# Performance work log

Hardware: AMD Instinct MI355X
Metric: run time of the kernel (lower is better)

The kernel has to match this reference:

```python
import jax, jax.numpy as jnp
import numpy as np

BN_EPS = 1e-5

def conv1x1(x, w, b):
    # x: [B,C,H,W], w: [O,C], b: [O]
    return jnp.einsum('bchw,oc->bohw', x, w) + b[None, :, None, None]

def bn_inf(x, gamma, beta, mean, var):
    inv = gamma / jnp.sqrt(var + BN_EPS)
    return (x - mean[None, :, None, None]) * inv[None, :, None, None] + beta[None, :, None, None]

def setup_inputs() -> dict:
    key = jax.random.key(0)
    ks = jax.random.split(key, 24)
    B, Fg, Fl, Fi = 8, 256, 256, 64
    H = W = 64
    c8 = Fi // 8
    d = {}
    d['g'] = jax.random.normal(ks[0], (B, Fg, H, W), jnp.float32)
    d['x'] = jax.random.normal(ks[1], (B, Fl, H, W), jnp.float32)
    # W_g: conv1x1 + BN
    d['Wg_w'] = jax.random.normal(ks[2], (Fi, Fg), jnp.float32) * (1.0 / np.sqrt(Fg))
    d['Wg_b'] = jax.random.normal(ks[3], (Fi,), jnp.float32) * 0.02
    d['bng_gamma'] = jax.random.uniform(ks[4], (Fi,), jnp.float32, 0.5, 1.5)
    d['bng_beta'] = jax.random.normal(ks[5], (Fi,), jnp.float32) * 0.1
    d['bng_mean'] = jax.random.normal(ks[6], (Fi,), jnp.float32) * 0.1
    d['bng_var'] = jax.random.uniform(ks[7], (Fi,), jnp.float32, 0.5, 1.5)
    # W_x: conv1x1 + BN
    d['Wx_w'] = jax.random.normal(ks[8], (Fi, Fl), jnp.float32) * (1.0 / np.sqrt(Fl))
    d['Wx_b'] = jax.random.normal(ks[9], (Fi,), jnp.float32) * 0.02
    d['bnx_gamma'] = jax.random.uniform(ks[10], (Fi,), jnp.float32, 0.5, 1.5)
    d['bnx_beta'] = jax.random.normal(ks[11], (Fi,), jnp.float32) * 0.1
    d['bnx_mean'] = jax.random.normal(ks[12], (Fi,), jnp.float32) * 0.1
    d['bnx_var'] = jax.random.uniform(ks[13], (Fi,), jnp.float32, 0.5, 1.5)
    # psi: conv1x1 (Fi->1) + BN(1) + sigmoid
    d['psi_w'] = jax.random.normal(ks[14], (1, Fi), jnp.float32) * (1.0 / np.sqrt(Fi))
    d['psi_b'] = jax.random.normal(ks[15], (1,), jnp.float32) * 0.02
    d['bnp_gamma'] = jax.random.uniform(ks[16], (1,), jnp.float32, 0.5, 1.5)
    d['bnp_beta'] = jax.random.normal(ks[17], (1,), jnp.float32) * 0.1
    d['bnp_mean'] = jax.random.normal(ks[18], (1,), jnp.float32) * 0.1
    d['bnp_var'] = jax.random.uniform(ks[19], (1,), jnp.float32, 0.5, 1.5)
    # PAM convs
    d['pb_w'] = jax.random.normal(ks[20], (c8, Fi), jnp.float32) * (1.0 / np.sqrt(Fi))
    d['pb_b'] = jnp.zeros((c8,), jnp.float32)
    d['pc_w'] = jax.random.normal(ks[21], (c8, Fi), jnp.float32) * (1.0 / np.sqrt(Fi))
    d['pc_b'] = jnp.zeros((c8,), jnp.float32)
    d['pd_w'] = jax.random.normal(ks[22], (Fi, Fi), jnp.float32) * (1.0 / np.sqrt(Fi))
    d['pd_b'] = jnp.zeros((Fi,), jnp.float32)
    # scalar gates (torch inits to 0; use small nonzero to exercise the path)
    d['alpha'] = jax.random.normal(ks[23], (1,), jnp.float32) * 0.05
    d['cam_beta'] = jax.random.normal(jax.random.fold_in(key, 99), (1,), jnp.float32) * 0.05
    return d

def _cam(psi, cam_beta):
    B, C, H, W = psi.shape
    feat = psi.reshape(B, C, H * W)                       # [B,C,HW]
    att = jnp.einsum('bcn,bdn->bcd', feat, feat)          # [B,C,C]
    att_new = jnp.max(att, axis=-1, keepdims=True) - att  # max-subtract trick
    att = jax.nn.softmax(att_new, axis=-1)
    out = jnp.einsum('bcd,bdn->bcn', att, feat).reshape(B, C, H, W)
    return cam_beta[0] * out + psi

def _pam(psi, pb_w, pb_b, pc_w, pc_b, pd_w, pd_b, alpha):
    B, C, H, W = psi.shape
    HW = H * W
    fb = conv1x1(psi, pb_w, pb_b).reshape(B, -1, HW)      # [B,C/8,HW]
    fc = conv1x1(psi, pc_w, pc_b).reshape(B, -1, HW)      # [B,C/8,HW]
    energy = jnp.einsum('bki,bkj->bij', fb, fc)           # [B,HW,HW]
    att = jax.nn.softmax(energy, axis=-1)
    fd = conv1x1(psi, pd_w, pd_b).reshape(B, C, HW)       # [B,C,HW]
    out = jnp.einsum('bcj,bij->bci', fd, att).reshape(B, C, H, W)
    return alpha[0] * out + psi

def reference(g, x, Wg_w, Wg_b, bng_gamma, bng_beta, bng_mean, bng_var,
              Wx_w, Wx_b, bnx_gamma, bnx_beta, bnx_mean, bnx_var,
              psi_w, psi_b, bnp_gamma, bnp_beta, bnp_mean, bnp_var,
              pb_w, pb_b, pc_w, pc_b, pd_w, pd_b, alpha, cam_beta):
    g1 = bn_inf(conv1x1(g, Wg_w, Wg_b), bng_gamma, bng_beta, bng_mean, bng_var)
    x1 = bn_inf(conv1x1(x, Wx_w, Wx_b), bnx_gamma, bnx_beta, bnx_mean, bnx_var)
    psi = jax.nn.relu(g1 + x1)                            # [B,F_int,H,W]
    cam = _cam(psi, cam_beta)
    pam = _pam(psi, pb_w, pb_b, pc_w, pc_b, pd_w, pd_b, alpha)
    gate = bn_inf(conv1x1(cam * pam, psi_w, psi_b), bnp_gamma, bnp_beta, bnp_mean, bnp_var)
    da = jax.nn.sigmoid(gate)                             # [B,1,H,W]
    return x * da
```

## Files before the change

### kernel.cpp

```cpp
#include <hip/hip_runtime.h>
#include <hip/hip_bf16.h>
#include <math.h>

#define BB 8
#define CIN 256
#define FI 64
#define HW 4096
#define C8 8
#define EPS 1e-5f

typedef __attribute__((ext_vector_type(8))) short bf16x8;
typedef __attribute__((ext_vector_type(4))) float f32x4;
typedef unsigned short u16;

static __device__ __forceinline__ u16 f2b(float x) {
    unsigned u = __builtin_bit_cast(unsigned, x);
    return (u16)((u + 0x8000u) >> 16);
}
static __device__ __forceinline__ unsigned pk2(float a, float b) {
    unsigned ua = __builtin_bit_cast(unsigned, a);
    unsigned ub = __builtin_bit_cast(unsigned, b);
    return ((ua + 0x8000u) >> 16) | ((ub + 0x8000u) & 0xffff0000u);
}
static __device__ __forceinline__ float b2f(u16 v) {
    return __builtin_bit_cast(float, ((unsigned)v) << 16);
}

__global__ __launch_bounds__(256) void k_prep(
    const float* __restrict__ Wg, const float* __restrict__ Wgb,
    const float* __restrict__ gg, const float* __restrict__ gbeta,
    const float* __restrict__ gm, const float* __restrict__ gv,
    const float* __restrict__ Wx, const float* __restrict__ Wxb,
    const float* __restrict__ xg, const float* __restrict__ xbeta,
    const float* __restrict__ xm, const float* __restrict__ xv,
    const float* __restrict__ pbw, const float* __restrict__ pbb,
    const float* __restrict__ pcw, const float* __restrict__ pcb,
    const float* __restrict__ pdw, const float* __restrict__ pdb,
    u16* __restrict__ Wp, float* __restrict__ Cp,
    u16* __restrict__ Wcat, float* __restrict__ bcat)
{
    const int gid = blockIdx.x * 256 + threadIdx.x;
    for (int idx = gid; idx < FI * 512; idx += 4096) {
        int o = idx >> 9, k = idx & 511;
        float s, w;
        if (k < 256) { s = gg[o] * rsqrtf(gv[o] + EPS); w = Wg[o * 256 + k]; }
        else         { s = xg[o] * rsqrtf(xv[o] + EPS); w = Wx[o * 256 + k - 256]; }
        Wp[idx] = f2b(w * s);
    }
    for (int idx = gid; idx < 80 * 64; idx += 4096) {
        int row = idx >> 6, col = idx & 63;
        float w;
        if (row < 8)       w = pbw[row * 64 + col];
        else if (row < 16) w = pcw[(row - 8) * 64 + col];
        else               w = pdw[(row - 16) * 64 + col];
        Wcat[idx] = f2b(w);
    }
    if (blockIdx.x == 0) {
        int tid = threadIdx.x;
        if (tid < FI) {
            float ig = gg[tid] * rsqrtf(gv[tid] + EPS);
            float ix = xg[tid] * rsqrtf(xv[tid] + EPS);
            Cp[tid] = (Wgb[tid] - gm[tid]) * ig + gbeta[tid]
                    + (Wxb[tid] - xm[tid]) * ix + xbeta[tid];
        }
        if (tid >= 64 && tid < 144) {
            int r = tid - 64;
            bcat[r] = (r < 8) ? pbb[r] : (r < 16 ? pcb[r - 8] : pdb[r - 16]);
        }
    }
}

__global__ __launch_bounds__(256) void k_psi(
    const float* __restrict__ g, const float* __restrict__ x,
    const u16* __restrict__ Wp, const float* __restrict__ Cp,
    const u16* __restrict__ Wcat, const float* __restrict__ bcat,
    u16* __restrict__ psiB, u16* __restrict__ psiLo,
    u16* __restrict__ fbcT, u16* __restrict__ fdB)
{
    const int tid  = threadIdx.x;
    const int lane = tid & 63;
    const int w    = tid >> 6;
    const int n    = lane & 15;
    const int quad = lane >> 4;
    const int b    = blockIdx.y;
    const int p0   = blockIdx.x * 64;

    __shared__ u16 InT[64][72];
    __shared__ u16 Tbc[64][16];

    f32x4 acc[4];
#pragma unroll
    for (int mt = 0; mt < 4; ++mt) acc[mt] = (f32x4){0.f, 0.f, 0.f, 0.f};

    for (int kc = 0; kc < 8; ++kc) {
        const float* src = (kc < 4) ? g : x;
        const int ch0 = (kc & 3) * 64;
        __syncthreads();
#pragma unroll
        for (int r = 0; r < 4; ++r) {
            int ch = (tid >> 4) + r * 16;
            int px = (tid & 15) * 4;
            float4 v = *(const float4*)&src[((size_t)b * CIN + ch0 + ch) * HW + p0 + px];
            InT[px][ch]     = f2b(v.x);
            InT[px + 1][ch] = f2b(v.y);
            InT[px + 2][ch] = f2b(v.z);
            InT[px + 3][ch] = f2b(v.w);
        }
        __syncthreads();
#pragma unroll
        for (int ks = 0; ks < 2; ++ks) {
            const int kglob = kc * 64 + ks * 32;
            bf16x8 bfrag = *(const bf16x8*)&InT[w * 16 + n][ks * 32 + quad * 8];
#pragma unroll
            for (int mt = 0; mt < 4; ++mt) {
                bf16x8 af = *(const bf16x8*)&Wp[(mt * 16 + n) * 512 + kglob + quad * 8];
                acc[mt] = __builtin_amdgcn_mfma_f32_16x16x32_bf16(
                              af, bfrag, acc[mt], 0, 0, 0);
            }
        }
    }

    float pv[4][4];
#pragma unroll
    for (int mt = 0; mt < 4; ++mt)
#pragma unroll
        for (int r = 0; r < 4; ++r) {
            int c = mt * 16 + quad * 4 + r;
            float v = acc[mt][r] + Cp[c];
            v = v > 0.f ? v : 0.f;
            pv[mt][r] = v;
            u16 hb = f2b(v);
            size_t idx = ((size_t)b * FI + c) * HW + p0 + w * 16 + n;
            psiB[idx]  = hb;
            psiLo[idx] = f2b(v - b2f(hb));
        }
    __syncthreads();
#pragma unroll
    for (int mt = 0; mt < 4; ++mt) {
        *(unsigned*)&InT[w * 16 + n][mt * 16 + quad * 4]     = pk2(pv[mt][0], pv[mt][1]);
        *(unsigned*)&InT[w * 16 + n][mt * 16 + quad * 4 + 2] = pk2(pv[mt][2], pv[mt][3]);
    }
    __syncthreads();

    f32x4 facc[5];
#pragma unroll
    for (int nt = 0; nt < 5; ++nt) facc[nt] = (f32x4){0.f, 0.f, 0.f, 0.f};
#pragma unroll
    for (int ks = 0; ks < 2; ++ks) {
        bf16x8 af = *(const bf16x8*)&InT[w * 16 + n][ks * 32 + quad * 8];
#pragma unroll
        for (int nt = 0; nt < 5; ++nt) {
            bf16x8 bf = *(const bf16x8*)&Wcat[(nt * 16 + n) * FI + ks * 32 + quad * 8];
            facc[nt] = __builtin_amdgcn_mfma_f32_16x16x32_bf16(af, bf, facc[nt], 0, 0, 0);
        }
    }
    __syncthreads();

    {
        float bias = bcat[n];
#pragma unroll
        for (int r = 0; r < 4; ++r)
            Tbc[w * 16 + quad * 4 + r][n] = f2b(facc[0][r] + bias);
    }
#pragma unroll
    for (int nt = 1; nt < 5; ++nt) {
        int ch = (nt - 1) * 16 + n;
        float bias = bcat[nt * 16 + n];
        *(unsigned*)&InT[ch][w * 16 + quad * 4]     = pk2(facc[nt][0] + bias, facc[nt][1] + bias);
        *(unsigned*)&InT[ch][w * 16 + quad * 4 + 2] = pk2(facc[nt][2] + bias, facc[nt][3] + bias);
    }
    __syncthreads();
    {
        int row = tid >> 2, part = tid & 3;
        uint2 v = *(const uint2*)&Tbc[row][part * 4];
        *(uint2*)&fbcT[((size_t)b * HW + p0 + row) * 16 + part * 4] = v;
    }
#pragma unroll
    for (int rep = 0; rep < 2; ++rep) {
        int t = rep * 256 + tid;
        int ch = t >> 3, seg = t & 7;
        bf16x8 v = *(const bf16x8*)&InT[ch][seg * 8];
        *(bf16x8*)&fdB[((size_t)b * FI + ch) * HW + p0 + seg * 8] = v;
    }
}

__global__ __launch_bounds__(256) void k_gram(
    const u16* __restrict__ psiB, const u16* __restrict__ psiLo,
    float* __restrict__ Gp)
{
    const int tid  = threadIdx.x;
    const int lane = tid & 63;
    const int w    = tid >> 6;
    const int n    = lane & 15;
    const int quad = lane >> 4;
    const int s    = blockIdx.x;
    const int b    = blockIdx.y;

    f32x4 acc[4];
#pragma unroll
    for (int nt = 0; nt < 4; ++nt) acc[nt] = (f32x4){0.f, 0.f, 0.f, 0.f};

    for (int ks = 0; ks < 4; ++ks) {
        const int k0 = s * 128 + ks * 32;
        const size_t ra = ((size_t)b * FI + w * 16 + n) * HW + k0 + quad * 8;
        bf16x8 ah = *(const bf16x8*)&psiB[ra];
        bf16x8 al = *(const bf16x8*)&psiLo[ra];
#pragma unroll
        for (int nt = 0; nt < 4; ++nt) {
            const size_t rb = ((size_t)b * FI + nt * 16 + n) * HW + k0 + quad * 8;
            bf16x8 bh = *(const bf16x8*)&psiB[rb];
            bf16x8 bl = *(const bf16x8*)&psiLo[rb];
            acc[nt] = __builtin_amdgcn_mfma_f32_16x16x32_bf16(ah, bh, acc[nt], 0, 0, 0);
            acc[nt] = __builtin_amdgcn_mfma_f32_16x16x32_bf16(ah, bl, acc[nt], 0, 0, 0);
            acc[nt] = __builtin_amdgcn_mfma_f32_16x16x32_bf16(al, bh, acc[nt], 0, 0, 0);
        }
    }
#pragma unroll
    for (int nt = 0; nt < 4; ++nt)
#pragma unroll
        for (int r = 0; r < 4; ++r) {
            int i = w * 16 + quad * 4 + r;
            Gp[(((size_t)s * 8 + b) * 64 + i) * 64 + nt * 16 + n] = acc[nt][r];
        }
}

__global__ __launch_bounds__(256) void k_camsm(
    const float* __restrict__ Gp, float* __restrict__ att)
{
    const int tid = threadIdx.x, d = tid & 63, ty = tid >> 6;
    const int b = blockIdx.x, grp = blockIdx.y;
#pragma unroll 1
    for (int rr = 0; rr < 4; ++rr) {
        int i = grp * 16 + ty * 4 + rr;
        float gsum = 0.f;
#pragma unroll 1
        for (int s = 0; s < 32; ++s) gsum += Gp[(((size_t)s * 8 + b) * 64 + i) * 64 + d];
        float M = gsum;
#pragma unroll
        for (int msk = 1; msk < 64; msk <<= 1) M = fmaxf(M, __shfl_xor(M, msk));
        float a = M - gsum;
        float m2 = a;
#pragma unroll
        for (int msk = 1; msk < 64; msk <<= 1) m2 = fmaxf(m2, __shfl_xor(m2, msk));
        float p = __expf(a - m2);
        float ssum = p;
#pragma unroll
        for (int msk = 1; msk < 64; msk <<= 1) ssum += __shfl_xor(ssum, msk);
        att[((size_t)b * 64 + i) * 64 + d] = p / ssum;
    }
}

__global__ __launch_bounds__(256) void k_pam(
    const u16* __restrict__ fbcT, const u16* __restrict__ fdB,
    u16* __restrict__ Opart, float* __restrict__ ml)
{
    const int tid  = threadIdx.x;
    const int lane = tid & 63;
    const int w    = tid >> 6;
    const int n    = lane & 15;
    const int quad = lane >> 4;
    const int b    = blockIdx.x;
    const int i0   = blockIdx.y * 64;
    const int p    = blockIdx.z;
    const int jstart = p * 32, jend = jstart + 32;

    __shared__ u16 Ks[68][8];
    __shared__ u16 Qs[64][32];
    __shared__ u16 Vs[64][72];
    __shared__ u16 Ps[4][16][72];

    for (int t = tid; t < 64 * 16; t += 256) ((unsigned*)Qs)[t] = 0u;
    if (tid < 16) ((unsigned*)&Ks[64][0])[tid] = 0u;
    __syncthreads();
    if (tid < 64)
        *(bf16x8*)&Qs[tid][0] = *(const bf16x8*)&fbcT[((size_t)b * HW + i0 + tid) * 16];
    __syncthreads();
    const bf16x8 qfrag = *(const bf16x8*)&Qs[w * 16 + n][quad * 8];

    const int kkey = tid >> 1, khalf = tid & 1;
    const int vch  = tid >> 3, vseg  = tid & 7;

    uint2 kreg = make_uint2(0u, 0u);
    bf16x8 vreg0, vreg1;
    {
        const int j0 = jstart * 64;
        if (tid < 128)
            kreg = *(const uint2*)&fbcT[((size_t)b * HW + j0 + kkey) * 16 + 8 + khalf * 4];
        vreg0 = *(const bf16x8*)&fdB[((size_t)b * FI + vch) * HW + j0 + vseg * 8];
        vreg1 = *(const bf16x8*)&fdB[((size_t)b * FI + 32 + vch) * HW + j0 + vseg * 8];
    }

    f32x4 oacc[4];
#pragma unroll
    for (int mt = 0; mt < 4; ++mt) oacc[mt] = (f32x4){0.f, 0.f, 0.f, 0.f};
    float m = -1e30f, l = 0.f;

    for (int jc = jstart; jc < jend; ++jc) {
        __syncthreads();
        if (tid < 128) *(uint2*)&Ks[kkey][khalf * 4] = kreg;
        *(bf16x8*)&Vs[vch][vseg * 8]      = vreg0;
        *(bf16x8*)&Vs[32 + vch][vseg * 8] = vreg1;
        if (jc + 1 < jend) {
            const int j0 = (jc + 1) * 64;
            if (tid < 128)
                kreg = *(const uint2*)&fbcT[((size_t)b * HW + j0 + kkey) * 16 + 8 + khalf * 4];
            vreg0 = *(const bf16x8*)&fdB[((size_t)b * FI + vch) * HW + j0 + vseg * 8];
            vreg1 = *(const bf16x8*)&fdB[((size_t)b * FI + 32 + vch) * HW + j0 + vseg * 8];
        }
        __syncthreads();

        f32x4 s[4];
#pragma unroll
        for (int mt = 0; mt < 4; ++mt) {
            bf16x8 af = *(const bf16x8*)&Ks[mt * 16 + n + quad][0];
            s[mt] = __builtin_amdgcn_mfma_f32_16x16x32_bf16(
                        af, qfrag, (f32x4){0.f, 0.f, 0.f, 0.f}, 0, 0, 0);
        }

        float cmax = -1e30f;
#pragma unroll
        for (int mt = 0; mt < 4; ++mt)
            cmax = fmaxf(cmax, fmaxf(fmaxf(s[mt][0], s[mt][1]),
                                     fmaxf(s[mt][2], s[mt][3])));
        cmax = fmaxf(cmax, __shfl_xor(cmax, 16));
        cmax = fmaxf(cmax, __shfl_xor(cmax, 32));
        float mnew  = fmaxf(m, cmax);
        float scale = __expf(m - mnew);
        float psum  = 0.f;
        unsigned pw[4][2];
#pragma unroll
        for (int mt = 0; mt < 4; ++mt) {
            float e0 = __expf(s[mt][0] - mnew), e1 = __expf(s[mt][1] - mnew);
            float e2 = __expf(s[mt][2] - mnew), e3 = __expf(s[mt][3] - mnew);
            psum += (e0 + e1) + (e2 + e3);
            pw[mt][0] = pk2(e0, e1);
            pw[mt][1] = pk2(e2, e3);
        }
        l = l * scale + psum;
        m = mnew;

#pragma unroll
        for (int mt = 0; mt < 4; ++mt)
            *(uint2*)&Ps[w][n][mt * 16 + quad * 4] = make_uint2(pw[mt][0], pw[mt][1]);
        asm volatile("s_waitcnt lgkmcnt(0)" ::: "memory");

#pragma unroll
        for (int mt = 0; mt < 4; ++mt) {
            oacc[mt][0] *= scale; oacc[mt][1] *= scale;
            oacc[mt][2] *= scale; oacc[mt][3] *= scale;
        }
#pragma unroll
        for (int k0 = 0; k0 < 2; ++k0) {
            bf16x8 pf = *(const bf16x8*)&Ps[w][n][k0 * 32 + quad * 8];
#pragma unroll
            for (int mt = 0; mt < 4; ++mt) {
                bf16x8 vf = *(const bf16x8*)&Vs[mt * 16 + n][k0 * 32 + quad * 8];
                oacc[mt] = __builtin_amdgcn_mfma_f32_16x16x32_bf16(
                               vf, pf, oacc[mt], 0, 0, 0);
            }
        }
    }

    l += __shfl_xor(l, 16);
    l += __shfl_xor(l, 32);
    const float rl = 1.f / l;
#pragma unroll
    for (int mt = 0; mt < 4; ++mt)
#pragma unroll
        for (int r = 0; r < 4; ++r) {
            int c = mt * 16 + quad * 4 + r;
            Opart[(((size_t)p * 8 + b) * FI + c) * HW + i0 + w * 16 + n] =
                f2b(oacc[mt][r] * rl);
        }
    if (quad == 0)
        ((float2*)ml)[((size_t)p * 8 + b) * HW + i0 + w * 16 + n] = make_float2(m, l);
}

__global__ __launch_bounds__(256) void k_final(
    const u16* __restrict__ psiB, const u16* __restrict__ psiLo,
    const float* __restrict__ att,
    const u16* __restrict__ Opart, const float* __restrict__ ml,
    const float* __restrict__ x,
    const float* __restrict__ psiw, const float* __restrict__ psib,
    const float* __restrict__ pg, const float* __restrict__ pbeta,
    const float* __restrict__ pm, const float* __restrict__ pv,
    const float* __restrict__ alpha, const float* __restrict__ camb,
    float* __restrict__ out)
{
    const int tid = threadIdx.x, tx = tid & 63, ty = tid >> 6;
    const int b = blockIdx.y, p0 = blockIdx.x * 64;
    __shared__ float tp[64][65];
    __shared__ float A[64][64];
    __shared__ float Zp[4][64];

#pragma unroll
    for (int r = 0; r < 16; ++r) {
        int c = ty * 16 + r;
        size_t idx = ((size_t)b * FI + c) * HW + p0 + tx;
        tp[c][tx] = b2f(psiB[idx]) + b2f(psiLo[idx]);
        A[c][tx]  = att[((size_t)b * 64 + c) * 64 + tx];
    }
    __syncthreads();

    float2 ml0 = ((const float2*)ml)[((size_t)0 * 8 + b) * HW + p0 + tx];
    float2 ml1 = ((const float2*)ml)[((size_t)1 * 8 + b) * HW + p0 + tx];
    float M  = fmaxf(ml0.x, ml1.x);
    float w0 = ml0.y * __expf(ml0.x - M);
    float w1 = ml1.y * __expf(ml1.x - M);
    float winv = 1.f / (w0 + w1);
    w0 *= winv; w1 *= winv;

    const float al = alpha[0], cb = camb[0];
    const int c0 = __builtin_amdgcn_readfirstlane(ty * 16);
    float acc[16];
#pragma unroll
    for (int i = 0; i < 16; ++i) acc[i] = 0.f;
#pragma unroll 16
    for (int d = 0; d < 64; ++d) {
        float v = tp[d][tx];
#pragma unroll
        for (int i = 0; i < 16; ++i) acc[i] += A[c0 + i][d] * v;
    }
    float z = 0.f;
#pragma unroll
    for (int i = 0; i < 16; ++i) {
        int c = c0 + i;
        float ps  = tp[c][tx];
        float cam = cb * acc[i] + ps;
        float oa = w0 * b2f(Opart[(((size_t)0 * 8 + b) * FI + c) * HW + p0 + tx])
                 + w1 * b2f(Opart[(((size_t)1 * 8 + b) * FI + c) * HW + p0 + tx]);
        float pam = al * oa + ps;
        z += psiw[c] * (cam * pam);
    }
    Zp[ty][tx] = z;
    __syncthreads();
    float zt = Zp[0][tx] + Zp[1][tx] + Zp[2][tx] + Zp[3][tx] + psib[0];
    float inv = pg[0] * rsqrtf(pv[0] + EPS);
    float gate = (zt - pm[0]) * inv + pbeta[0];
    float da = 1.f / (1.f + __expf(-gate));

#pragma unroll 8
    for (int r = 0; r < 64; ++r) {
        int cl = ty + 4 * r;
        size_t idx = ((size_t)b * CIN + cl) * HW + p0 + tx;
        out[idx] = x[idx] * da;
    }
}

extern "C" void kernel_launch(void* const* d_in, const int* in_sizes, int n_in,
                              void* d_out, int out_size, void* d_ws, size_t ws_size,
                              hipStream_t stream)
{
    const float* g     = (const float*)d_in[0];
    const float* x     = (const float*)d_in[1];
    const float* Wg_w  = (const float*)d_in[2];
    const float* Wg_b  = (const float*)d_in[3];
    const float* bng_g = (const float*)d_in[4];
    const float* bng_b = (const float*)d_in[5];
    const float* bng_m = (const float*)d_in[6];
    const float* bng_v = (const float*)d_in[7];
    const float* Wx_w  = (const float*)d_in[8];
    const float* Wx_b  = (const float*)d_in[9];
    const float* bnx_g = (const float*)d_in[10];
    const float* bnx_b = (const float*)d_in[11];
    const float* bnx_m = (const float*)d_in[12];
    const float* bnx_v = (const float*)d_in[13];
    const float* psi_w = (const float*)d_in[14];
    const float* psi_b = (const float*)d_in[15];
    const float* bnp_g = (const float*)d_in[16];
    const float* bnp_b = (const float*)d_in[17];
    const float* bnp_m = (const float*)d_in[18];
    const float* bnp_v = (const float*)d_in[19];
    const float* pb_w  = (const float*)d_in[20];
    const float* pb_b  = (const float*)d_in[21];
    const float* pc_w  = (const float*)d_in[22];
    const float* pc_b  = (const float*)d_in[23];
    const float* pd_w  = (const float*)d_in[24];
    const float* pd_b  = (const float*)d_in[25];
    const float* alpha = (const float*)d_in[26];
    const float* camb  = (const float*)d_in[27];
    float* out = (float*)d_out;

    float* ws   = (float*)d_ws;
    u16*  psiB  = (u16*)(ws);
    u16*  psiLo = (u16*)(ws + 1048576);
    u16*  fbcT  = (u16*)(ws + 2097152);
    u16*  fdB   = (u16*)(ws + 2359296);
    float* att  = ws + 3407872;
    u16*  Wp    = (u16*)(ws + 3440640);
    float* Cp   = ws + 3457024;
    u16*  Wcat  = (u16*)(ws + 3457088);
    float* bcat = ws + 3459648;
    float* mlws = ws + 3459744;
    float* Gp   = ws + 3590816;
    u16*  Opart = (u16*)(ws + 3590816);

    k_prep<<<dim3(16), 256, 0, stream>>>(Wg_w, Wg_b, bng_g, bng_b, bng_m, bng_v,
                                         Wx_w, Wx_b, bnx_g, bnx_b, bnx_m, bnx_v,
                                         pb_w, pb_b, pc_w, pc_b, pd_w, pd_b,
                                         Wp, Cp, Wcat, bcat);
    k_psi<<<dim3(64, 8), 256, 0, stream>>>(g, x, Wp, Cp, Wcat, bcat,
                                           psiB, psiLo, fbcT, fdB);
    k_gram<<<dim3(32, 8), 256, 0, stream>>>(psiB, psiLo, Gp);
    k_camsm<<<dim3(8, 4), 256, 0, stream>>>(Gp, att);
    k_pam<<<dim3(8, 64, 2), 256, 0, stream>>>(fbcT, fdB, Opart, mlws);
    k_final<<<dim3(64, 8), 256, 0, stream>>>(psiB, psiLo, att, Opart, mlws, x,
                                             psi_w, psi_b, bnp_g, bnp_b, bnp_m, bnp_v,
                                             alpha, camb, out);
}
```

Baseline: 297.6 us.

## Use base-2 softmax with lazy rescaling and hardware bf16 pack conversions

```diff
diff --git a/kernel.cpp b/kernel.cpp
--- a/kernel.cpp
+++ b/kernel.cpp
@@ -8,6 +8,7 @@
 #define HW 4096
 #define C8 8
 #define EPS 1e-5f
+#define LOG2E 1.4426950408889634f
 
 typedef __attribute__((ext_vector_type(8))) short bf16x8;
 typedef __attribute__((ext_vector_type(4))) float f32x4;
@@ -21,6 +22,11 @@
     unsigned ua = __builtin_bit_cast(unsigned, a);
     unsigned ub = __builtin_bit_cast(unsigned, b);
     return ((ua + 0x8000u) >> 16) | ((ub + 0x8000u) & 0xffff0000u);
+}
+static __device__ __forceinline__ unsigned cvtpk(float a, float b) {
+    unsigned r;
+    asm("v_cvt_pk_bf16_f32 %0, %1, %2" : "=v"(r) : "v"(a), "v"(b));
+    return r;
 }
 static __device__ __forceinline__ float b2f(u16 v) {
     return __builtin_bit_cast(float, ((unsigned)v) << 16);
@@ -50,7 +56,7 @@
     for (int idx = gid; idx < 80 * 64; idx += 4096) {
         int row = idx >> 6, col = idx & 63;
         float w;
-        if (row < 8)       w = pbw[row * 64 + col];
+        if (row < 8)       w = pbw[row * 64 + col] * LOG2E;
         else if (row < 16) w = pcw[(row - 8) * 64 + col];
         else               w = pdw[(row - 16) * 64 + col];
         Wcat[idx] = f2b(w);
@@ -65,7 +71,8 @@
         }
         if (tid >= 64 && tid < 144) {
             int r = tid - 64;
-            bcat[r] = (r < 8) ? pbb[r] : (r < 16 ? pcb[r - 8] : pdb[r - 16]);
+            float bv = (r < 8) ? pbb[r] * LOG2E : (r < 16 ? pcb[r - 8] : pdb[r - 16]);
+            bcat[r] = bv;
         }
     }
 }
@@ -137,8 +144,8 @@
     __syncthreads();
 #pragma unroll
     for (int mt = 0; mt < 4; ++mt) {
-        *(unsigned*)&InT[w * 16 + n][mt * 16 + quad * 4]     = pk2(pv[mt][0], pv[mt][1]);
-        *(unsigned*)&InT[w * 16 + n][mt * 16 + quad * 4 + 2] = pk2(pv[mt][2], pv[mt][3]);
+        *(unsigned*)&InT[w * 16 + n][mt * 16 + quad * 4]     = cvtpk(pv[mt][0], pv[mt][1]);
+        *(unsigned*)&InT[w * 16 + n][mt * 16 + quad * 4 + 2] = cvtpk(pv[mt][2], pv[mt][3]);
     }
     __syncthreads();
 
@@ -166,8 +173,8 @@
     for (int nt = 1; nt < 5; ++nt) {
         int ch = (nt - 1) * 16 + n;
         float bias = bcat[nt * 16 + n];
-        *(unsigned*)&InT[ch][w * 16 + quad * 4]     = pk2(facc[nt][0] + bias, facc[nt][1] + bias);
-        *(unsigned*)&InT[ch][w * 16 + quad * 4 + 2] = pk2(facc[nt][2] + bias, facc[nt][3] + bias);
+        *(unsigned*)&InT[ch][w * 16 + quad * 4]     = cvtpk(facc[nt][0] + bias, facc[nt][1] + bias);
+        *(unsigned*)&InT[ch][w * 16 + quad * 4 + 2] = cvtpk(facc[nt][2] + bias, facc[nt][3] + bias);
     }
     __syncthreads();
     {
@@ -280,14 +287,16 @@
     const int kkey = tid >> 1, khalf = tid & 1;
     const int vch  = tid >> 3, vseg  = tid & 7;
 
+    const u16* kp  = fbcT + ((size_t)b * HW + jstart * 64) * 16;
+    const u16* vp  = fdB + (size_t)b * FI * HW + jstart * 64;
+
     uint2 kreg = make_uint2(0u, 0u);
     bf16x8 vreg0, vreg1;
     {
-        const int j0 = jstart * 64;
         if (tid < 128)
-            kreg = *(const uint2*)&fbcT[((size_t)b * HW + j0 + kkey) * 16 + 8 + khalf * 4];
-        vreg0 = *(const bf16x8*)&fdB[((size_t)b * FI + vch) * HW + j0 + vseg * 8];
-        vreg1 = *(const bf16x8*)&fdB[((size_t)b * FI + 32 + vch) * HW + j0 + vseg * 8];
+            kreg = *(const uint2*)(kp + (size_t)kkey * 16 + 8 + khalf * 4);
+        vreg0 = *(const bf16x8*)(vp + (size_t)vch * HW + vseg * 8);
+        vreg1 = *(const bf16x8*)(vp + (size_t)(32 + vch) * HW + vseg * 8);
     }
 
     f32x4 oacc[4];
@@ -301,11 +310,12 @@
         *(bf16x8*)&Vs[vch][vseg * 8]      = vreg0;
         *(bf16x8*)&Vs[32 + vch][vseg * 8] = vreg1;
         if (jc + 1 < jend) {
-            const int j0 = (jc + 1) * 64;
+            kp += 64 * 16;
+            vp += 64;
             if (tid < 128)
-                kreg = *(const uint2*)&fbcT[((size_t)b * HW + j0 + kkey) * 16 + 8 + khalf * 4];
-            vreg0 = *(const bf16x8*)&fdB[((size_t)b * FI + vch) * HW + j0 + vseg * 8];
-            vreg1 = *(const bf16x8*)&fdB[((size_t)b * FI + 32 + vch) * HW + j0 + vseg * 8];
+                kreg = *(const uint2*)(kp + (size_t)kkey * 16 + 8 + khalf * 4);
+            vreg0 = *(const bf16x8*)(vp + (size_t)vch * HW + vseg * 8);
+            vreg1 = *(const bf16x8*)(vp + (size_t)(32 + vch) * HW + vseg * 8);
         }
         __syncthreads();
 
@@ -324,31 +334,38 @@
                                      fmaxf(s[mt][2], s[mt][3])));
         cmax = fmaxf(cmax, __shfl_xor(cmax, 16));
         cmax = fmaxf(cmax, __shfl_xor(cmax, 32));
-        float mnew  = fmaxf(m, cmax);
-        float scale = __expf(m - mnew);
-        float psum  = 0.f;
+
+        if (__any(cmax > m + 8.f)) {
+            float mnew  = fmaxf(m, cmax);
+            float scale = __builtin_amdgcn_exp2f(m - mnew);
+            l *= scale;
+#pragma unroll
+            for (int mt = 0; mt < 4; ++mt) {
+                oacc[mt][0] *= scale; oacc[mt][1] *= scale;
+                oacc[mt][2] *= scale; oacc[mt][3] *= scale;
+            }
+            m = mnew;
+        }
+
+        float psum = 0.f;
         unsigned pw[4][2];
 #pragma unroll
         for (int mt = 0; mt < 4; ++mt) {
-            float e0 = __expf(s[mt][0] - mnew), e1 = __expf(s[mt][1] - mnew);
-            float e2 = __expf(s[mt][2] - mnew), e3 = __expf(s[mt][3] - mnew);
+            float e0 = __builtin_amdgcn_exp2f(s[mt][0] - m);
+            float e1 = __builtin_amdgcn_exp2f(s[mt][1] - m);
+            float e2 = __builtin_amdgcn_exp2f(s[mt][2] - m);
+            float e3 = __builtin_amdgcn_exp2f(s[mt][3] - m);
             psum += (e0 + e1) + (e2 + e3);
-            pw[mt][0] = pk2(e0, e1);
-            pw[mt][1] = pk2(e2, e3);
-        }
-        l = l * scale + psum;
-        m = mnew;
+            pw[mt][0] = cvtpk(e0, e1);
+            pw[mt][1] = cvtpk(e2, e3);
+        }
+        l += psum;
 
 #pragma unroll
         for (int mt = 0; mt < 4; ++mt)
             *(uint2*)&Ps[w][n][mt * 16 + quad * 4] = make_uint2(pw[mt][0], pw[mt][1]);
         asm volatile("s_waitcnt lgkmcnt(0)" ::: "memory");
 
-#pragma unroll
-        for (int mt = 0; mt < 4; ++mt) {
-            oacc[mt][0] *= scale; oacc[mt][1] *= scale;
-            oacc[mt][2] *= scale; oacc[mt][3] *= scale;
-        }
 #pragma unroll
         for (int k0 = 0; k0 < 2; ++k0) {
             bf16x8 pf = *(const bf16x8*)&Ps[w][n][k0 * 32 + quad * 8];
@@ -405,8 +422,8 @@
     float2 ml0 = ((const float2*)ml)[((size_t)0 * 8 + b) * HW + p0 + tx];
     float2 ml1 = ((const float2*)ml)[((size_t)1 * 8 + b) * HW + p0 + tx];
     float M  = fmaxf(ml0.x, ml1.x);
-    float w0 = ml0.y * __expf(ml0.x - M);
-    float w1 = ml1.y * __expf(ml1.x - M);
+    float w0 = ml0.y * __builtin_amdgcn_exp2f(ml0.x - M);
+    float w1 = ml1.y * __builtin_amdgcn_exp2f(ml1.x - M);
     float winv = 1.f / (w0 + w1);
     w0 *= winv; w1 *= winv;
 
```

Result: no change. 292.4 us (-1.7%).
